# Performance work log

Hardware: AMD Instinct MI355X
Metric: run time of the kernel (lower is better)

## Reference

```python
import jax, jax.numpy as jnp
import numpy as np

B, T, D, H, C = 128, 512, 128, 64, 45

def _p(key, shape, scale):
    return jax.random.normal(key, shape, dtype=jnp.float32) * scale

def setup_inputs() -> dict:
    key = jax.random.key(0)
    ks = jax.random.split(key, 10)
    sD, sH, s2H = 1.0 / np.sqrt(D), 1.0 / np.sqrt(H), 1.0 / np.sqrt(2 * H)
    b = jnp.zeros((4 * H,), jnp.float32)
    return {
        "x": jax.random.normal(ks[0], (B, T, D), dtype=jnp.float32),
        "W1f": _p(ks[1], (D, 4 * H), sD), "U1f": _p(ks[2], (H, 4 * H), sH), "b1f": b,
        "W1b": _p(ks[3], (D, 4 * H), sD), "U1b": _p(ks[4], (H, 4 * H), sH), "b1b": b,
        "W2f": _p(ks[5], (2 * H, 4 * H), s2H), "U2f": _p(ks[6], (H, 4 * H), sH), "b2f": b,
        "W2b": _p(ks[7], (2 * H, 4 * H), s2H), "U2b": _p(ks[8], (H, 4 * H), sH), "b2b": b,
        "Wd": _p(ks[9], (2 * H, C), s2H), "bd": jnp.zeros((C,), jnp.float32),
    }

def _lstm_dir(x, W, U, b, reverse):
    # Keras LSTM with activation=relu, recurrent_activation=sigmoid, gate order [i,f,c,o].
    if reverse:
        x = x[:, ::-1, :]
    xz = jnp.einsum('btd,dg->btg', x, W) + b  # precompute input projections [B,T,4H]
    h0 = jnp.zeros((x.shape[0], H), x.dtype)

    def step(carry, z_t):
        h, c = carry
        z = z_t + h @ U  # [B,4H]
        i, f, g, o = jnp.split(z, 4, axis=-1)
        c = jax.nn.sigmoid(f) * c + jax.nn.sigmoid(i) * jax.nn.relu(g)
        h = jax.nn.sigmoid(o) * jax.nn.relu(c)
        return (h, c), h

    _, hs = jax.lax.scan(step, (h0, h0), jnp.swapaxes(xz, 0, 1))  # [T,B,H]
    hs = jnp.swapaxes(hs, 0, 1)  # [B,T,H]
    return hs[:, ::-1, :] if reverse else hs

def reference(x, W1f, U1f, b1f, W1b, U1b, b1b, W2f, U2f, b2f, W2b, U2b, b2b, Wd, bd):
    h1 = jnp.concatenate([_lstm_dir(x, W1f, U1f, b1f, False),
                          _lstm_dir(x, W1b, U1b, b1b, True)], axis=-1)   # [B,T,2H]
    h2 = jnp.concatenate([_lstm_dir(h1, W2f, U2f, b2f, False),
                          _lstm_dir(h1, W2b, U2b, b2b, True)], axis=-1)  # [B,T,2H]
    logits = h2 @ Wd + bd  # [B,T,C]
    return jax.nn.softmax(logits, axis=-1)
```

## Files before the change

### kernel.cpp

```cpp
#include <hip/hip_runtime.h>

#define TT 512
#define NB 128
#define DD 128
#define HH 64
#define CC 45

__device__ __forceinline__ float sigf(float x) { return 1.0f / (1.0f + __expf(-x)); }

#define LDS_BAR() asm volatile("s_waitcnt lgkmcnt(0)\n\ts_barrier" ::: "memory")

#define QP_XOR1(x) __int_as_float(__builtin_amdgcn_mov_dpp(__float_as_int(x), 0xB1, 0xF, 0xF, true))
#define QP_XOR2(x) __int_as_float(__builtin_amdgcn_mov_dpp(__float_as_int(x), 0x4E, 0xF, 0xF, true))

__device__ __forceinline__ ushort f2bf(float x) {
    uint u = __float_as_uint(x);
    u += 0x7FFFu + ((u >> 16) & 1u);
    return (ushort)(u >> 16);
}
__device__ __forceinline__ float bf2f(ushort h) { return __uint_as_float(((uint)h) << 16); }

typedef short short8 __attribute__((ext_vector_type(8)));
typedef float f32x4 __attribute__((ext_vector_type(4)));

__global__ __launch_bounds__(256, 2) void gemm_xz_mfma2(
    const float* __restrict__ A, const float* __restrict__ Wf,
    const float* __restrict__ Wb, const float* __restrict__ biasf,
    const float* __restrict__ biasb, float* __restrict__ Cout)
{
    __shared__ ushort Wh[128][136];
    __shared__ ushort Wl[128][136];

    const int tid = threadIdx.x;
    const int n0  = blockIdx.x * 128;
    const int m0  = blockIdx.y * 128;
    const float* W   = (n0 < 256) ? Wf : Wb;
    const float* bia = (n0 < 256) ? biasf : biasb;
    const int nc0 = n0 & 255;

    {
        const int r  = tid >> 1;
        const int cb = (tid & 1) * 64;
        #pragma unroll
        for (int i = 0; i < 16; ++i) {
            const int c = cb + i * 4;
            const float4 wv = *(const float4*)&W[(size_t)r * 256 + nc0 + c];
            const ushort h0 = (ushort)(__float_as_uint(wv.x) >> 16);
            const ushort h1 = (ushort)(__float_as_uint(wv.y) >> 16);
            const ushort h2 = (ushort)(__float_as_uint(wv.z) >> 16);
            const ushort h3 = (ushort)(__float_as_uint(wv.w) >> 16);
            Wh[c + 0][r] = h0; Wl[c + 0][r] = f2bf(wv.x - bf2f(h0));
            Wh[c + 1][r] = h1; Wl[c + 1][r] = f2bf(wv.y - bf2f(h1));
            Wh[c + 2][r] = h2; Wl[c + 2][r] = f2bf(wv.z - bf2f(h2));
            Wh[c + 3][r] = h3; Wl[c + 3][r] = f2bf(wv.w - bf2f(h3));
        }
    }
    __syncthreads();

    const int lane = tid & 63, wv_ = tid >> 6;
    const int fr = lane & 15, fg = lane >> 4;

    f32x4 acc[2][8];
    #pragma unroll
    for (int ms = 0; ms < 2; ++ms)
        #pragma unroll
        for (int nt = 0; nt < 8; ++nt) acc[ms][nt] = (f32x4){0.f, 0.f, 0.f, 0.f};

    #pragma unroll
    for (int ks = 0; ks < 4; ++ks) {
        const int kb = ks * 32 + fg * 8;
        short8 ah[2], al[2];
        #pragma unroll
        for (int ms = 0; ms < 2; ++ms) {
            const float* ap = &A[(size_t)(m0 + wv_ * 32 + ms * 16 + fr) * 128 + kb];
            const float4 va = *(const float4*)ap;
            const float4 vb = *(const float4*)(ap + 4);
            float v[8] = {va.x, va.y, va.z, va.w, vb.x, vb.y, vb.z, vb.w};
            #pragma unroll
            for (int j = 0; j < 8; ++j) {
                const ushort hj = (ushort)(__float_as_uint(v[j]) >> 16);
                ah[ms][j] = (short)hj;
                al[ms][j] = (short)f2bf(v[j] - bf2f(hj));
            }
        }
        #pragma unroll
        for (int nt = 0; nt < 8; ++nt) {
            const short8 bh = *(const short8*)&Wh[nt * 16 + fr][kb];
            const short8 bl = *(const short8*)&Wl[nt * 16 + fr][kb];
            acc[0][nt] = __builtin_amdgcn_mfma_f32_16x16x32_bf16(ah[0], bh, acc[0][nt], 0, 0, 0);
            acc[0][nt] = __builtin_amdgcn_mfma_f32_16x16x32_bf16(ah[0], bl, acc[0][nt], 0, 0, 0);
            acc[0][nt] = __builtin_amdgcn_mfma_f32_16x16x32_bf16(al[0], bh, acc[0][nt], 0, 0, 0);
            acc[1][nt] = __builtin_amdgcn_mfma_f32_16x16x32_bf16(ah[1], bh, acc[1][nt], 0, 0, 0);
            acc[1][nt] = __builtin_amdgcn_mfma_f32_16x16x32_bf16(ah[1], bl, acc[1][nt], 0, 0, 0);
            acc[1][nt] = __builtin_amdgcn_mfma_f32_16x16x32_bf16(al[1], bh, acc[1][nt], 0, 0, 0);
        }
    }

    #pragma unroll
    for (int nt = 0; nt < 8; ++nt) {
        const float bb = bia[nc0 + nt * 16 + fr];
        #pragma unroll
        for (int ms = 0; ms < 2; ++ms) {
            #pragma unroll
            for (int j = 0; j < 4; ++j) {
                const int mg = m0 + wv_ * 32 + ms * 16 + fg * 4 + j;
                Cout[(size_t)mg * 512 + n0 + nt * 16 + fr] = acc[ms][nt][j] + bb;
            }
        }
    }
}

__global__
__attribute__((amdgpu_flat_work_group_size(512, 512), amdgpu_waves_per_eu(1, 2)))
void lstm_rec_qp(
    const float* __restrict__ xz, const float* __restrict__ Uf,
    const float* __restrict__ Ubw, float* __restrict__ hout)
{
    const int b   = blockIdx.x & 127;
    const int dir = blockIdx.x >> 7;
    const int tid = threadIdx.x;
    const int w    = tid >> 6;
    const int lane = tid & 63;
    const int gate = lane & 3;
    const int colL = (lane >> 2) & 7;
    const int kh   = lane >> 5;
    const int col  = w * 8 + colL;
    const int gcol = gate * 64 + col;
    const float* U = dir ? Ubw : Uf;

    __shared__ float hbuf[2][64];

    const float* Ug = U + (size_t)(kh * 32) * 256 + gcol;
    float u0  = Ug[ 0*256], u1  = Ug[ 1*256], u2  = Ug[ 2*256], u3  = Ug[ 3*256];
    float u4  = Ug[ 4*256], u5  = Ug[ 5*256], u6  = Ug[ 6*256], u7  = Ug[ 7*256];
    float u8  = Ug[ 8*256], u9  = Ug[ 9*256], u10 = Ug[10*256], u11 = Ug[11*256];
    float u12 = Ug[12*256], u13 = Ug[13*256], u14 = Ug[14*256], u15 = Ug[15*256];
    float u16 = Ug[16*256], u17 = Ug[17*256], u18 = Ug[18*256], u19 = Ug[19*256];
    float u20 = Ug[20*256], u21 = Ug[21*256], u22 = Ug[22*256], u23 = Ug[23*256];
    float u24 = Ug[24*256], u25 = Ug[25*256], u26 = Ug[26*256], u27 = Ug[27*256];
    float u28 = Ug[28*256], u29 = Ug[29*256], u30 = Ug[30*256], u31 = Ug[31*256];
    asm volatile("" : "+v"(u0),"+v"(u1),"+v"(u2),"+v"(u3),
                      "+v"(u4),"+v"(u5),"+v"(u6),"+v"(u7));
    asm volatile("" : "+v"(u8),"+v"(u9),"+v"(u10),"+v"(u11),
                      "+v"(u12),"+v"(u13),"+v"(u14),"+v"(u15));
    asm volatile("" : "+v"(u16),"+v"(u17),"+v"(u18),"+v"(u19),
                      "+v"(u20),"+v"(u21),"+v"(u22),"+v"(u23));
    asm volatile("" : "+v"(u24),"+v"(u25),"+v"(u26),"+v"(u27),
                      "+v"(u28),"+v"(u29),"+v"(u30),"+v"(u31));

    if (tid < 64) hbuf[0][tid] = 0.f;
    float c = 0.f;
    __syncthreads();

    const float* xzb = xz + (size_t)b * TT * 512 + (size_t)dir * 256 + gcol;
    float*       hob = hout + (size_t)b * TT * 128 + (size_t)dir * 64 + col;

    int trow = dir ? (TT - 1) : 0;
    const int ts = dir ? -1 : 1;
    float xc = xzb[(size_t)trow * 512];
    float x1 = xzb[(size_t)(trow + ts) * 512];

    for (int s = 0; s < TT; ++s) {
        const int p = s & 1;
        float x2 = 0.f;
        if (s + 2 < TT) x2 = xzb[(size_t)(trow + 2 * ts) * 512];

        float a0 = 0.f, a1 = 0.f, a2 = 0.f, a3 = 0.f;
#define ACC(J, A,B,C,D) { const float4 hv = *(const float4*)&hbuf[p][kh*32 + 4*(J)]; \
        a0 = __fmaf_rn(hv.x, A, a0); a1 = __fmaf_rn(hv.y, B, a1); \
        a2 = __fmaf_rn(hv.z, C, a2); a3 = __fmaf_rn(hv.w, D, a3); }
        ACC(0,u0 ,u1 ,u2 ,u3 ) ACC(1,u4 ,u5 ,u6 ,u7 )
        ACC(2,u8 ,u9 ,u10,u11) ACC(3,u12,u13,u14,u15)
        ACC(4,u16,u17,u18,u19) ACC(5,u20,u21,u22,u23)
        ACC(6,u24,u25,u26,u27) ACC(7,u28,u29,u30,u31)
#undef ACC
        float part = (a0 + a1) + (a2 + a3);

        part += __shfl_xor(part, 32);
        const float z = xc + part;

        const float a = (gate == 2) ? fmaxf(z, 0.f) : sigf(z);

        const float b0 = QP_XOR1(a);
        const float b1 = QP_XOR2(a);
        const float b2 = QP_XOR2(b0);
        const float ai = (gate == 0) ? a : (gate == 1) ? b0 : (gate == 2) ? b1 : b2;
        const float af = (gate == 1) ? a : (gate == 0) ? b0 : (gate == 3) ? b1 : b2;
        const float ag = (gate == 2) ? a : (gate == 3) ? b0 : (gate == 0) ? b1 : b2;
        const float ao = (gate == 3) ? a : (gate == 2) ? b0 : (gate == 1) ? b1 : b2;

        c = af * c + ai * ag;
        const float h = ao * fmaxf(c, 0.f);

        if ((lane & 0x23) == 0) {
            hbuf[p ^ 1][col] = h;
            hob[(size_t)trow * 128] = h;
        }

        LDS_BAR();

        xc = x1; x1 = x2;
        trow += ts;
    }
}

__global__ __launch_bounds__(256) void dense_softmax(
    const float* __restrict__ h2, const float* __restrict__ Wd,
    const float* __restrict__ bd, float* __restrict__ out)
{
    __shared__ float Wl[128 * 45];
    __shared__ float bl[48];
    __shared__ float hrow[4][128];
    const int tid = threadIdx.x;
    for (int i = tid; i < 128 * 45; i += 256) Wl[i] = Wd[i];
    if (tid < 45) bl[tid] = bd[tid];
    __syncthreads();

    const int w = tid >> 6, l = tid & 63;
    const size_t row0 = (size_t)blockIdx.x * 64;
    for (int rr = 0; rr < 16; ++rr) {
        const size_t m = row0 + (size_t)rr * 4 + w;
        const float2 hv = *(const float2*)&h2[m * 128 + l * 2];
        hrow[w][l * 2] = hv.x;
        hrow[w][l * 2 + 1] = hv.y;
        __syncthreads();
        float lg = -3.0e38f;
        if (l < CC) {
            lg = bl[l];
            #pragma unroll 8
            for (int k = 0; k < 128; ++k) lg = __fmaf_rn(hrow[w][k], Wl[k * 45 + l], lg);
        }
        float mx = lg;
        #pragma unroll
        for (int off = 32; off >= 1; off >>= 1) mx = fmaxf(mx, __shfl_xor(mx, off));
        const float e = (l < CC) ? __expf(lg - mx) : 0.f;
        float sm = e;
        #pragma unroll
        for (int off = 32; off >= 1; off >>= 1) sm += __shfl_xor(sm, off);
        if (l < CC) out[m * 45 + l] = e / sm;
        __syncthreads();
    }
}

extern "C" void kernel_launch(void* const* d_in, const int* in_sizes, int n_in,
                              void* d_out, int out_size, void* d_ws, size_t ws_size,
                              hipStream_t stream)
{
    const float* x   = (const float*)d_in[0];
    const float* W1f = (const float*)d_in[1];
    const float* U1f = (const float*)d_in[2];
    const float* b1f = (const float*)d_in[3];
    const float* W1b = (const float*)d_in[4];
    const float* U1b = (const float*)d_in[5];
    const float* b1b = (const float*)d_in[6];
    const float* W2f = (const float*)d_in[7];
    const float* U2f = (const float*)d_in[8];
    const float* b2f = (const float*)d_in[9];
    const float* W2b = (const float*)d_in[10];
    const float* U2b = (const float*)d_in[11];
    const float* b2b = (const float*)d_in[12];
    const float* Wd  = (const float*)d_in[13];
    const float* bd  = (const float*)d_in[14];

    float* xz = (float*)d_ws;
    float* h  = (float*)((char*)d_ws + (size_t)65536 * 512 * 4);

    const dim3 gemm_grid(4, 512);
    const dim3 rec_grid(256);
    const dim3 dense_grid(1024);

    gemm_xz_mfma2<<<gemm_grid, dim3(256), 0, stream>>>(x, W1f, W1b, b1f, b1b, xz);
    lstm_rec_qp<<<rec_grid, dim3(512), 0, stream>>>(xz, U1f, U1b, h);
    gemm_xz_mfma2<<<gemm_grid, dim3(256), 0, stream>>>(h, W2f, W2b, b2f, b2b, xz);
    lstm_rec_qp<<<rec_grid, dim3(512), 0, stream>>>(xz, U2f, U2b, h);
    dense_softmax<<<dense_grid, dim3(256), 0, stream>>>(h, Wd, bd, (float*)d_out);
}
```

Before: 603.5 us.

## Batch 16 sequences per block and compute LSTM recurrence with split-bf16 MFMA

Replaces the per-sequence FMA recurrence kernel (256 blocks of 512 threads, one sequence each) with a kernel where each 256-thread block handles 16 batch rows. Each step's h@U is computed with bf16 MFMA, using a hi/lo split of h and U to keep near-fp32 accuracy. This amortizes the per-step barrier and latency chain across 16 sequences and uses matrix cores. The grid shrinks to 16 blocks, though, so only 16 CUs are busy and the serial per-step latency of six chained MFMAs plus gate math may dominate.

Measured after the change: 1.201 ms. 1.99x slower.

```diff
diff --git a/kernel.cpp b/kernel.cpp
--- a/kernel.cpp
+++ b/kernel.cpp
@@ -10,9 +10,6 @@
 
 #define LDS_BAR() asm volatile("s_waitcnt lgkmcnt(0)\n\ts_barrier" ::: "memory")
 
-#define QP_XOR1(x) __int_as_float(__builtin_amdgcn_mov_dpp(__float_as_int(x), 0xB1, 0xF, 0xF, true))
-#define QP_XOR2(x) __int_as_float(__builtin_amdgcn_mov_dpp(__float_as_int(x), 0x4E, 0xF, 0xF, true))
-
 __device__ __forceinline__ ushort f2bf(float x) {
     uint u = __float_as_uint(x);
     u += 0x7FFFu + ((u >> 16) & 1u);
@@ -22,6 +19,22 @@
 
 typedef short short8 __attribute__((ext_vector_type(8)));
 typedef float f32x4 __attribute__((ext_vector_type(4)));
+
+__device__ __forceinline__ uint pkbf(float a, float b) {
+    uint r; asm("v_cvt_pk_bf16_f32 %0, %1, %2" : "=v"(r) : "v"(a), "v"(b)); return r;
+}
+__device__ __forceinline__ float lo2f(uint p) { return __uint_as_float(p << 16); }
+__device__ __forceinline__ float hi2f(uint p) { return __uint_as_float(p & 0xFFFF0000u); }
+__device__ __forceinline__ short8 mk8(uint a, uint b, uint c, uint d) {
+    union { uint u[4]; short8 s; } x; x.u[0]=a; x.u[1]=b; x.u[2]=c; x.u[3]=d; return x.s;
+}
+#define SPLIT8(o0,o1,o2,o3,o4,o5,o6,o7, H, L) { \
+    const uint h0_ = pkbf(o0,o1), h1_ = pkbf(o2,o3), h2_ = pkbf(o4,o5), h3_ = pkbf(o6,o7); \
+    const uint l0_ = pkbf((o0) - lo2f(h0_), (o1) - hi2f(h0_)); \
+    const uint l1_ = pkbf((o2) - lo2f(h1_), (o3) - hi2f(h1_)); \
+    const uint l2_ = pkbf((o4) - lo2f(h2_), (o5) - hi2f(h2_)); \
+    const uint l3_ = pkbf((o6) - lo2f(h3_), (o7) - hi2f(h3_)); \
+    H = mk8(h0_,h1_,h2_,h3_); L = mk8(l0_,l1_,l2_,l3_); }
 
 __global__ __launch_bounds__(256, 2) void gemm_xz_mfma2(
     const float* __restrict__ A, const float* __restrict__ Wf,
@@ -110,97 +123,114 @@
     }
 }
 
-__global__
-__attribute__((amdgpu_flat_work_group_size(512, 512), amdgpu_waves_per_eu(1, 2)))
-void lstm_rec_qp(
+__global__ __launch_bounds__(256, 1) void lstm_rec_mm(
     const float* __restrict__ xz, const float* __restrict__ Uf,
     const float* __restrict__ Ubw, float* __restrict__ hout)
 {
-    const int b   = blockIdx.x & 127;
-    const int dir = blockIdx.x >> 7;
+    const int bid = blockIdx.x;
+    const int dir = bid >> 3;
+    const int b0  = (bid & 7) << 4;
     const int tid = threadIdx.x;
     const int w    = tid >> 6;
     const int lane = tid & 63;
-    const int gate = lane & 3;
-    const int colL = (lane >> 2) & 7;
-    const int kh   = lane >> 5;
-    const int col  = w * 8 + colL;
-    const int gcol = gate * 64 + col;
+    const int fr = lane & 15;
+    const int fg = lane >> 4;
     const float* U = dir ? Ubw : Uf;
 
-    __shared__ float hbuf[2][64];
-
-    const float* Ug = U + (size_t)(kh * 32) * 256 + gcol;
-    float u0  = Ug[ 0*256], u1  = Ug[ 1*256], u2  = Ug[ 2*256], u3  = Ug[ 3*256];
-    float u4  = Ug[ 4*256], u5  = Ug[ 5*256], u6  = Ug[ 6*256], u7  = Ug[ 7*256];
-    float u8  = Ug[ 8*256], u9  = Ug[ 9*256], u10 = Ug[10*256], u11 = Ug[11*256];
-    float u12 = Ug[12*256], u13 = Ug[13*256], u14 = Ug[14*256], u15 = Ug[15*256];
-    float u16 = Ug[16*256], u17 = Ug[17*256], u18 = Ug[18*256], u19 = Ug[19*256];
-    float u20 = Ug[20*256], u21 = Ug[21*256], u22 = Ug[22*256], u23 = Ug[23*256];
-    float u24 = Ug[24*256], u25 = Ug[25*256], u26 = Ug[26*256], u27 = Ug[27*256];
-    float u28 = Ug[28*256], u29 = Ug[29*256], u30 = Ug[30*256], u31 = Ug[31*256];
-    asm volatile("" : "+v"(u0),"+v"(u1),"+v"(u2),"+v"(u3),
-                      "+v"(u4),"+v"(u5),"+v"(u6),"+v"(u7));
-    asm volatile("" : "+v"(u8),"+v"(u9),"+v"(u10),"+v"(u11),
-                      "+v"(u12),"+v"(u13),"+v"(u14),"+v"(u15));
-    asm volatile("" : "+v"(u16),"+v"(u17),"+v"(u18),"+v"(u19),
-                      "+v"(u20),"+v"(u21),"+v"(u22),"+v"(u23));
-    asm volatile("" : "+v"(u24),"+v"(u25),"+v"(u26),"+v"(u27),
-                      "+v"(u28),"+v"(u29),"+v"(u30),"+v"(u31));
-
-    if (tid < 64) hbuf[0][tid] = 0.f;
-    float c = 0.f;
+    __shared__ float hbuf[2][16][68];
+
+#define LDU(g, kh, H, L) short8 H, L; { \
+    const float* up = U + (size_t)((kh)*32 + fg*8) * 256 + (g)*64 + w*16 + fr; \
+    const float v0 = up[0*256], v1 = up[1*256], v2 = up[2*256], v3 = up[3*256]; \
+    const float v4 = up[4*256], v5 = up[5*256], v6 = up[6*256], v7 = up[7*256]; \
+    SPLIT8(v0,v1,v2,v3,v4,v5,v6,v7, H, L) }
+    LDU(0,0, uh00, ul00)  LDU(0,1, uh01, ul01)
+    LDU(1,0, uh10, ul10)  LDU(1,1, uh11, ul11)
+    LDU(2,0, uh20, ul20)  LDU(2,1, uh21, ul21)
+    LDU(3,0, uh30, ul30)  LDU(3,1, uh31, ul31)
+#undef LDU
+
+    for (int i = tid; i < 2 * 16 * 68; i += 256) ((float*)hbuf)[i] = 0.f;
+    f32x4 cst = (f32x4){0.f, 0.f, 0.f, 0.f};
     __syncthreads();
 
-    const float* xzb = xz + (size_t)b * TT * 512 + (size_t)dir * 256 + gcol;
-    float*       hob = hout + (size_t)b * TT * 128 + (size_t)dir * 64 + col;
+    const float* xr0 = xz + (size_t)(b0 + fg*4 + 0) * TT * 512 + dir * 256 + w*16 + fr;
+    const float* xr1 = xz + (size_t)(b0 + fg*4 + 1) * TT * 512 + dir * 256 + w*16 + fr;
+    const float* xr2 = xz + (size_t)(b0 + fg*4 + 2) * TT * 512 + dir * 256 + w*16 + fr;
+    const float* xr3 = xz + (size_t)(b0 + fg*4 + 3) * TT * 512 + dir * 256 + w*16 + fr;
+    float* hb0 = hout + (size_t)(b0 + fg*4 + 0) * TT * 128 + dir * 64 + w*16 + fr;
+    float* hb1 = hout + (size_t)(b0 + fg*4 + 1) * TT * 128 + dir * 64 + w*16 + fr;
+    float* hb2 = hout + (size_t)(b0 + fg*4 + 2) * TT * 128 + dir * 64 + w*16 + fr;
+    float* hb3 = hout + (size_t)(b0 + fg*4 + 3) * TT * 128 + dir * 64 + w*16 + fr;
 
     int trow = dir ? (TT - 1) : 0;
     const int ts = dir ? -1 : 1;
-    float xc = xzb[(size_t)trow * 512];
-    float x1 = xzb[(size_t)(trow + ts) * 512];
-
+
+    f32x4 xcI, xcF, xcG, xcO;
+    {
+        const size_t o = (size_t)trow * 512;
+        xcI = (f32x4){xr0[o+  0], xr1[o+  0], xr2[o+  0], xr3[o+  0]};
+        xcF = (f32x4){xr0[o+ 64], xr1[o+ 64], xr2[o+ 64], xr3[o+ 64]};
+        xcG = (f32x4){xr0[o+128], xr1[o+128], xr2[o+128], xr3[o+128]};
+        xcO = (f32x4){xr0[o+192], xr1[o+192], xr2[o+192], xr3[o+192]};
+    }
+
+    int p = 0;
     for (int s = 0; s < TT; ++s) {
-        const int p = s & 1;
-        float x2 = 0.f;
-        if (s + 2 < TT) x2 = xzb[(size_t)(trow + 2 * ts) * 512];
-
-        float a0 = 0.f, a1 = 0.f, a2 = 0.f, a3 = 0.f;
-#define ACC(J, A,B,C,D) { const float4 hv = *(const float4*)&hbuf[p][kh*32 + 4*(J)]; \
-        a0 = __fmaf_rn(hv.x, A, a0); a1 = __fmaf_rn(hv.y, B, a1); \
-        a2 = __fmaf_rn(hv.z, C, a2); a3 = __fmaf_rn(hv.w, D, a3); }
-        ACC(0,u0 ,u1 ,u2 ,u3 ) ACC(1,u4 ,u5 ,u6 ,u7 )
-        ACC(2,u8 ,u9 ,u10,u11) ACC(3,u12,u13,u14,u15)
-        ACC(4,u16,u17,u18,u19) ACC(5,u20,u21,u22,u23)
-        ACC(6,u24,u25,u26,u27) ACC(7,u28,u29,u30,u31)
-#undef ACC
-        float part = (a0 + a1) + (a2 + a3);
-
-        part += __shfl_xor(part, 32);
-        const float z = xc + part;
-
-        const float a = (gate == 2) ? fmaxf(z, 0.f) : sigf(z);
-
-        const float b0 = QP_XOR1(a);
-        const float b1 = QP_XOR2(a);
-        const float b2 = QP_XOR2(b0);
-        const float ai = (gate == 0) ? a : (gate == 1) ? b0 : (gate == 2) ? b1 : b2;
-        const float af = (gate == 1) ? a : (gate == 0) ? b0 : (gate == 3) ? b1 : b2;
-        const float ag = (gate == 2) ? a : (gate == 3) ? b0 : (gate == 0) ? b1 : b2;
-        const float ao = (gate == 3) ? a : (gate == 2) ? b0 : (gate == 1) ? b1 : b2;
-
-        c = af * c + ai * ag;
-        const float h = ao * fmaxf(c, 0.f);
-
-        if ((lane & 0x23) == 0) {
-            hbuf[p ^ 1][col] = h;
-            hob[(size_t)trow * 128] = h;
-        }
+        const int pn = p ^ 1;
+        const int trn = trow + ts;
+
+        f32x4 xnI, xnF, xnG, xnO;
+        if (s + 1 < TT) {
+            const size_t o = (size_t)trn * 512;
+            xnI = (f32x4){xr0[o+  0], xr1[o+  0], xr2[o+  0], xr3[o+  0]};
+            xnF = (f32x4){xr0[o+ 64], xr1[o+ 64], xr2[o+ 64], xr3[o+ 64]};
+            xnG = (f32x4){xr0[o+128], xr1[o+128], xr2[o+128], xr3[o+128]};
+            xnO = (f32x4){xr0[o+192], xr1[o+192], xr2[o+192], xr3[o+192]};
+        } else {
+            xnI = xnF = xnG = xnO = (f32x4){0.f, 0.f, 0.f, 0.f};
+        }
+
+        const float* hrow = &hbuf[p][fr][0];
+        const float4 hA = *(const float4*)&hrow[fg*8];
+        const float4 hB = *(const float4*)&hrow[fg*8 + 4];
+        const float4 hC = *(const float4*)&hrow[32 + fg*8];
+        const float4 hD = *(const float4*)&hrow[32 + fg*8 + 4];
+        short8 ah0, al0, ah1, al1;
+        SPLIT8(hA.x,hA.y,hA.z,hA.w, hB.x,hB.y,hB.z,hB.w, ah0, al0)
+        SPLIT8(hC.x,hC.y,hC.z,hC.w, hD.x,hD.y,hD.z,hD.w, ah1, al1)
+
+        f32x4 azi = xcI, azf = xcF, azg = xcG, azo = xcO;
+#define MM(dst, H0, H1, L0, L1) \
+        dst = __builtin_amdgcn_mfma_f32_16x16x32_bf16(ah0, H0, dst, 0,0,0); \
+        dst = __builtin_amdgcn_mfma_f32_16x16x32_bf16(ah1, H1, dst, 0,0,0); \
+        dst = __builtin_amdgcn_mfma_f32_16x16x32_bf16(ah0, L0, dst, 0,0,0); \
+        dst = __builtin_amdgcn_mfma_f32_16x16x32_bf16(ah1, L1, dst, 0,0,0); \
+        dst = __builtin_amdgcn_mfma_f32_16x16x32_bf16(al0, H0, dst, 0,0,0); \
+        dst = __builtin_amdgcn_mfma_f32_16x16x32_bf16(al1, H1, dst, 0,0,0);
+        MM(azi, uh00, uh01, ul00, ul01)
+        MM(azf, uh10, uh11, ul10, ul11)
+        MM(azg, uh20, uh21, ul20, ul21)
+        MM(azo, uh30, uh31, ul30, ul31)
+#undef MM
+
+#define GATE_J(j, hbp) { \
+        const float gi = sigf(azi[j]); \
+        const float gf = sigf(azf[j]); \
+        const float gg = fmaxf(azg[j], 0.f); \
+        const float go = sigf(azo[j]); \
+        cst[j] = gf * cst[j] + gi * gg; \
+        const float hj = go * fmaxf(cst[j], 0.f); \
+        hbuf[pn][fg*4 + j][w*16 + fr] = hj; \
+        hbp[(size_t)trow * 128] = hj; }
+        GATE_J(0, hb0) GATE_J(1, hb1) GATE_J(2, hb2) GATE_J(3, hb3)
+#undef GATE_J
 
         LDS_BAR();
 
-        xc = x1; x1 = x2;
-        trow += ts;
+        xcI = xnI; xcF = xnF; xcG = xnG; xcO = xnO;
+        trow = trn;
+        p = pn;
     }
 }
 
@@ -266,12 +296,12 @@
     float* h  = (float*)((char*)d_ws + (size_t)65536 * 512 * 4);
 
     const dim3 gemm_grid(4, 512);
-    const dim3 rec_grid(256);
+    const dim3 rec_grid(16);
     const dim3 dense_grid(1024);
 
     gemm_xz_mfma2<<<gemm_grid, dim3(256), 0, stream>>>(x, W1f, W1b, b1f, b1b, xz);
-    lstm_rec_qp<<<rec_grid, dim3(512), 0, stream>>>(xz, U1f, U1b, h);
+    lstm_rec_mm<<<rec_grid, dim3(256), 0, stream>>>(xz, U1f, U1b, h);
     gemm_xz_mfma2<<<gemm_grid, dim3(256), 0, stream>>>(h, W2f, W2b, b2f, b2b, xz);
-    lstm_rec_qp<<<rec_grid, dim3(512), 0, stream>>>(xz, U2f, U2b, h);
+    lstm_rec_mm<<<rec_grid, dim3(256), 0, stream>>>(xz, U2f, U2b, h);
     dense_softmax<<<dense_grid, dim3(256), 0, stream>>>(h, Wd, bd, (float*)d_out);
 }
```

## Split LSTM recurrence K-dim across 4 lanes with 1024-thread blocks

Applied to the files above, without the earlier changes.

The recurrent kernel now uses 1024 threads per block and splits the 64-wide hidden dot product four ways across quad lanes instead of two ways. Each lane holds 16 U weights instead of 32, which shortens the serial FMA chain per timestep. The partial-sum reduction moves to two quad DPP ops, and the gate exchange moves to cross-row shuffles. In exchange, each barrier now spans twice as many waves, and the gate gather uses slower ds_swizzle/bpermute shuffles instead of DPP.

Result: slower. 708.0 us (+17.3%).

```diff
diff --git a/kernel.cpp b/kernel.cpp
--- a/kernel.cpp
+++ b/kernel.cpp
@@ -110,9 +110,7 @@
     }
 }
 
-__global__
-__attribute__((amdgpu_flat_work_group_size(512, 512), amdgpu_waves_per_eu(1, 2)))
-void lstm_rec_qp(
+__global__ __launch_bounds__(1024, 1) void lstm_rec_qd(
     const float* __restrict__ xz, const float* __restrict__ Uf,
     const float* __restrict__ Ubw, float* __restrict__ hout)
 {
@@ -121,32 +119,24 @@
     const int tid = threadIdx.x;
     const int w    = tid >> 6;
     const int lane = tid & 63;
-    const int gate = lane & 3;
-    const int colL = (lane >> 2) & 7;
-    const int kh   = lane >> 5;
-    const int col  = w * 8 + colL;
+    const int kq   = lane & 3;
+    const int colL = (lane >> 2) & 3;
+    const int gate = lane >> 4;
+    const int col  = w * 4 + colL;
     const int gcol = gate * 64 + col;
     const float* U = dir ? Ubw : Uf;
 
     __shared__ float hbuf[2][64];
 
-    const float* Ug = U + (size_t)(kh * 32) * 256 + gcol;
-    float u0  = Ug[ 0*256], u1  = Ug[ 1*256], u2  = Ug[ 2*256], u3  = Ug[ 3*256];
-    float u4  = Ug[ 4*256], u5  = Ug[ 5*256], u6  = Ug[ 6*256], u7  = Ug[ 7*256];
-    float u8  = Ug[ 8*256], u9  = Ug[ 9*256], u10 = Ug[10*256], u11 = Ug[11*256];
-    float u12 = Ug[12*256], u13 = Ug[13*256], u14 = Ug[14*256], u15 = Ug[15*256];
-    float u16 = Ug[16*256], u17 = Ug[17*256], u18 = Ug[18*256], u19 = Ug[19*256];
-    float u20 = Ug[20*256], u21 = Ug[21*256], u22 = Ug[22*256], u23 = Ug[23*256];
-    float u24 = Ug[24*256], u25 = Ug[25*256], u26 = Ug[26*256], u27 = Ug[27*256];
-    float u28 = Ug[28*256], u29 = Ug[29*256], u30 = Ug[30*256], u31 = Ug[31*256];
-    asm volatile("" : "+v"(u0),"+v"(u1),"+v"(u2),"+v"(u3),
-                      "+v"(u4),"+v"(u5),"+v"(u6),"+v"(u7));
-    asm volatile("" : "+v"(u8),"+v"(u9),"+v"(u10),"+v"(u11),
-                      "+v"(u12),"+v"(u13),"+v"(u14),"+v"(u15));
-    asm volatile("" : "+v"(u16),"+v"(u17),"+v"(u18),"+v"(u19),
-                      "+v"(u20),"+v"(u21),"+v"(u22),"+v"(u23));
-    asm volatile("" : "+v"(u24),"+v"(u25),"+v"(u26),"+v"(u27),
-                      "+v"(u28),"+v"(u29),"+v"(u30),"+v"(u31));
+    const float* Ug = U + (size_t)(kq * 16) * 256 + gcol;
+    float u0  = Ug[0 * 256],  u1  = Ug[1 * 256],  u2  = Ug[2 * 256],  u3  = Ug[3 * 256];
+    float u4  = Ug[4 * 256],  u5  = Ug[5 * 256],  u6  = Ug[6 * 256],  u7  = Ug[7 * 256];
+    float u8  = Ug[8 * 256],  u9  = Ug[9 * 256],  u10 = Ug[10 * 256], u11 = Ug[11 * 256];
+    float u12 = Ug[12 * 256], u13 = Ug[13 * 256], u14 = Ug[14 * 256], u15 = Ug[15 * 256];
+    asm volatile("" : "+v"(u0), "+v"(u1), "+v"(u2), "+v"(u3),
+                      "+v"(u4), "+v"(u5), "+v"(u6), "+v"(u7),
+                      "+v"(u8), "+v"(u9), "+v"(u10), "+v"(u11),
+                      "+v"(u12), "+v"(u13), "+v"(u14), "+v"(u15));
 
     if (tid < 64) hbuf[0][tid] = 0.f;
     float c = 0.f;
@@ -165,25 +155,30 @@
         float x2 = 0.f;
         if (s + 2 < TT) x2 = xzb[(size_t)(trow + 2 * ts) * 512];
 
+        const float4 h0 = *(const float4*)&hbuf[p][kq * 16 + 0];
+        const float4 h1 = *(const float4*)&hbuf[p][kq * 16 + 4];
+        const float4 h2 = *(const float4*)&hbuf[p][kq * 16 + 8];
+        const float4 h3 = *(const float4*)&hbuf[p][kq * 16 + 12];
         float a0 = 0.f, a1 = 0.f, a2 = 0.f, a3 = 0.f;
-#define ACC(J, A,B,C,D) { const float4 hv = *(const float4*)&hbuf[p][kh*32 + 4*(J)]; \
-        a0 = __fmaf_rn(hv.x, A, a0); a1 = __fmaf_rn(hv.y, B, a1); \
-        a2 = __fmaf_rn(hv.z, C, a2); a3 = __fmaf_rn(hv.w, D, a3); }
-        ACC(0,u0 ,u1 ,u2 ,u3 ) ACC(1,u4 ,u5 ,u6 ,u7 )
-        ACC(2,u8 ,u9 ,u10,u11) ACC(3,u12,u13,u14,u15)
-        ACC(4,u16,u17,u18,u19) ACC(5,u20,u21,u22,u23)
-        ACC(6,u24,u25,u26,u27) ACC(7,u28,u29,u30,u31)
-#undef ACC
+        a0 = __fmaf_rn(h0.x, u0,  a0); a1 = __fmaf_rn(h0.y, u1,  a1);
+        a2 = __fmaf_rn(h0.z, u2,  a2); a3 = __fmaf_rn(h0.w, u3,  a3);
+        a0 = __fmaf_rn(h1.x, u4,  a0); a1 = __fmaf_rn(h1.y, u5,  a1);
+        a2 = __fmaf_rn(h1.z, u6,  a2); a3 = __fmaf_rn(h1.w, u7,  a3);
+        a0 = __fmaf_rn(h2.x, u8,  a0); a1 = __fmaf_rn(h2.y, u9,  a1);
+        a2 = __fmaf_rn(h2.z, u10, a2); a3 = __fmaf_rn(h2.w, u11, a3);
+        a0 = __fmaf_rn(h3.x, u12, a0); a1 = __fmaf_rn(h3.y, u13, a1);
+        a2 = __fmaf_rn(h3.z, u14, a2); a3 = __fmaf_rn(h3.w, u15, a3);
         float part = (a0 + a1) + (a2 + a3);
 
-        part += __shfl_xor(part, 32);
+        part += QP_XOR1(part);
+        part += QP_XOR2(part);
         const float z = xc + part;
 
         const float a = (gate == 2) ? fmaxf(z, 0.f) : sigf(z);
 
-        const float b0 = QP_XOR1(a);
-        const float b1 = QP_XOR2(a);
-        const float b2 = QP_XOR2(b0);
+        const float b0 = __shfl_xor(a, 16);
+        const float b1 = __shfl_xor(a, 32);
+        const float b2 = __shfl_xor(b0, 32);
         const float ai = (gate == 0) ? a : (gate == 1) ? b0 : (gate == 2) ? b1 : b2;
         const float af = (gate == 1) ? a : (gate == 0) ? b0 : (gate == 3) ? b1 : b2;
         const float ag = (gate == 2) ? a : (gate == 3) ? b0 : (gate == 0) ? b1 : b2;
@@ -192,7 +187,7 @@
         c = af * c + ai * ag;
         const float h = ao * fmaxf(c, 0.f);
 
-        if ((lane & 0x23) == 0) {
+        if ((lane & 0x33) == 0) {
             hbuf[p ^ 1][col] = h;
             hob[(size_t)trow * 128] = h;
         }
@@ -270,8 +265,8 @@
     const dim3 dense_grid(1024);
 
     gemm_xz_mfma2<<<gemm_grid, dim3(256), 0, stream>>>(x, W1f, W1b, b1f, b1b, xz);
-    lstm_rec_qp<<<rec_grid, dim3(512), 0, stream>>>(xz, U1f, U1b, h);
+    lstm_rec_qd<<<rec_grid, dim3(1024), 0, stream>>>(xz, U1f, U1b, h);
     gemm_xz_mfma2<<<gemm_grid, dim3(256), 0, stream>>>(h, W2f, W2b, b2f, b2b, xz);
-    lstm_rec_qp<<<rec_grid, dim3(512), 0, stream>>>(xz, U2f, U2b, h);
+    lstm_rec_qd<<<rec_grid, dim3(1024), 0, stream>>>(xz, U2f, U2b, h);
     dense_softmax<<<dense_grid, dim3(256), 0, stream>>>(h, Wd, bd, (float*)d_out);
 }
```
